# Optimization experiments

Hardware: AMD Instinct MI355X
Metric: run time of the kernel (lower is better)

Reference implementation:

```python
import jax, jax.numpy as jnp
import numpy as np

DT = np.float32(1.0 / 262.0)   # 1 / NUM_TRADING_DAYS
ETA = np.float32(1e-6)
T = 131072


def setup_inputs() -> dict:
    key = jax.random.key(0)
    k1, k2, k3 = jax.random.split(key, 3)
    return {
        "observations": jax.random.normal(k1, (T,), jnp.float32) * 0.01,
        "garch": jax.random.normal(k2, (T,), jnp.float32) * 0.01,
        "carma": jax.random.normal(k3, (T, 2), jnp.float32) * 0.01,
        "w0": jnp.zeros((3,), jnp.float32),
        "P0": jnp.eye(3, dtype=jnp.float32) * 0.01,
        "b0": jnp.float32(0.1),
        "b1": jnp.float32(0.05),
        "a1": jnp.float32(0.5),
        "kappa": jnp.float32(0.01),
        "theta": jnp.float32(0.01),
        "xi": jnp.float32(0.01),
        "rho": jnp.float32(0.01),
    }


def _ekf(observations, garch, carma, w0, P0, b0, b1, a1, kappa, theta, xi, rho):
    kap = jax.nn.softplus(kappa)
    xi_ = jax.nn.softplus(xi)
    rho_ = jnp.tanh(rho)
    zero = jnp.float32(0.0)
    phi_vec = jnp.stack([zero, b0, b1])            # emission coefficients
    phi_row = phi_vec * DT                          # 1x3 phi matrix (as a row)
    I3 = jnp.eye(3, dtype=jnp.float32)

    def step(carry, xs):
        w, P = carry
        obs, g0, c0, c1 = xs
        # --- transition Jacobian psi(w) and drift ---
        th = jax.nn.softplus(theta + g0)
        term = kap * th * jnp.clip(jnp.exp(-w[0]), 0.0, 1.0)
        term = jnp.where(jnp.isnan(term), zero, term)  # nan guard from torch code
        Psi = (I3.at[0, 0].set(1.0 - term)
                  .at[1, 2].set(DT)
                  .at[2, 2].set(1.0 - a1 * DT))
        # --- process noise R(w) ---
        sigma = jnp.exp(w[0] / 2)
        cross = sigma * xi_ * rho_
        R = (jnp.zeros((3, 3), jnp.float32)
                .at[0, 0].set(xi_ ** 2)
                .at[0, 2].set(cross)
                .at[2, 0].set(cross)
                .at[2, 2].set(sigma ** 2)) * DT + I3 * ETA
        # --- state prediction ---
        psi_vec = jnp.stack([term + xi_ ** 2 / 2 - kap, w[2] + c0, -a1 * w[2] + c1])
        w_pred = w + psi_vec * DT
        P_pred = Psi @ P @ Psi.T + R
        P_pred = (P_pred + P_pred.T) / 2 + I3 * ETA
        # --- observation prediction: Q = phi P phi^T + S(w_pred) then sym + ETA*I ---
        x_pred = jnp.dot(phi_vec, w_pred) * DT
        sig2p = jnp.exp(w_pred[0])                 # sigma(w_pred)^2
        Q = phi_row @ P_pred @ phi_row + (sig2p * DT + ETA) + ETA  # scalar
        # --- Kalman gain and posterior update ---
        K = (P_pred @ phi_row) / Q                 # (3,)
        innov = obs - x_pred
        w_post = w_pred + K * innov
        P_post = (I3 - jnp.outer(K, phi_row)) @ P_pred
        P_post = (P_post + P_post.T) / 2 + I3 * ETA
        return (w_post, P_post), (w_post, x_pred)

    xs = (observations, garch, carma[:, 0], carma[:, 1])
    (_, _), (w_seq, x_seq) = jax.lax.scan(step, (w0, P0), xs)
    # [T, 4]: predicted observation and posterior state per step
    return jnp.concatenate([x_seq[:, None], w_seq], axis=1)


def reference(observations, garch, carma, w0, P0, b0, b1, a1, kappa, theta, xi, rho):
    return _ekf(observations, garch, carma, w0, P0, b0, b1, a1, kappa, theta, xi, rho)
```

## Files before the change

kernel.cpp:

```cpp
#include <hip/hip_runtime.h>
#include <math.h>


#define DTV (1.0f/262.0f)
#define C_COARSE 256
#define C_FINE 1024
#define C_SUPER 64
#define NF 4
#define STR 17
#define UPF_A 32
#define UPF_B 8
#define UPF_F 8
#define ETA1 1e-6f
#define ETA2C 2e-6f

__device__ __forceinline__ float softplus_f(float x) {
    return fmaxf(x, 0.0f) + log1pf(__expf(-fabsf(x)));
}

struct EKFConsts {
    float d2, d2sq, f1, f2, cw, f2d2, ffd;
    float invd2, dtd2i, f1sq, f1f2, f2sq, cwDT;
};

__device__ __forceinline__ void load_consts(EKFConsts& c,
    const float* pb0, const float* pb1, const float* pa1,
    const float* pkappa, const float* pxi)
{
    float b0 = pb0[0], b1 = pb1[0], a1 = pa1[0];
    float kap = softplus_f(pkappa[0]);
    float xi_ = softplus_f(pxi[0]);
    float xi2 = xi_ * xi_;
    c.d2    = 1.0f - a1 * DTV;
    c.d2sq  = c.d2 * c.d2;
    c.f1    = b0 * DTV;
    c.f2    = b1 * DTV;
    c.cw    = 0.5f * xi2 - kap;
    c.f2d2  = c.f2 * c.d2;
    c.ffd   = fmaf(c.f1, DTV, c.f2d2);
    c.invd2 = 1.0f / c.d2;
    c.dtd2i = DTV * c.invd2;
    c.f1sq  = c.f1 * c.f1;
    c.f1f2  = c.f1 * c.f2;
    c.f2sq  = c.f2 * c.f2;
    c.cwDT  = c.cw * DTV;
}

__device__ __forceinline__ float poly_exp(float w) {
    return fmaf(w, fmaf(w, fmaf(w, (1.0f/6.0f), 0.5f), 1.0f), 1.0f);
}
__device__ __forceinline__ float poly_expn(float w) {
    float p = fmaf(w, -(1.0f/6.0f), 0.5f);
    p = fmaf(w, p, -1.0f);
    return fminf(fmaf(w, p, 1.0f), 1.0f);
}

__device__ __forceinline__ void mobius_apply(const float* h,
    float& p11, float& p12, float& p22)
{
    float X11 = fmaf(h[0], p11, fmaf(h[4], p12, h[8]));
    float X12 = fmaf(h[0], p12, fmaf(h[4], p22, h[12]));
    float X21 = fmaf(h[1], p11, fmaf(h[5], p12, h[9]));
    float X22 = fmaf(h[1], p12, fmaf(h[5], p22, h[13]));
    float Y11 = fmaf(h[2], p11, fmaf(h[6], p12, h[10]));
    float Y12 = fmaf(h[2], p12, fmaf(h[6], p22, h[14]));
    float Y21 = fmaf(h[3], p11, fmaf(h[7], p12, h[11]));
    float Y22 = fmaf(h[3], p12, fmaf(h[7], p22, h[15]));
    float det = fmaf(Y11, Y22, -Y12 * Y21);
    float idet = __builtin_amdgcn_rcpf(det);
    float P11 = fmaf(X11, Y22, -X12 * Y21) * idet;
    float P12 = fmaf(X12, Y11, -X11 * Y12) * idet;
    float P21 = fmaf(X21, Y22, -X22 * Y21) * idet;
    float P22 = fmaf(X22, Y11, -X21 * Y12) * idet;
    p11 = P11; p12 = 0.5f * (P12 + P21); p22 = P22;
}

__device__ __forceinline__ void mat4_mul(float* C, const float* A, const float* B)
{
    #pragma unroll
    for (int col = 0; col < 4; ++col) {
        #pragma unroll
        for (int row = 0; row < 4; ++row) {
            float s = A[0*4+row] * B[col*4+0];
            s = fmaf(A[1*4+row], B[col*4+1], s);
            s = fmaf(A[2*4+row], B[col*4+2], s);
            s = fmaf(A[3*4+row], B[col*4+3], s);
            C[col*4+row] = s;
        }
    }
}

__global__ void ekf_pack_kt(const float* __restrict__ g,
                            const float* __restrict__ ptheta,
                            const float* __restrict__ pkappa,
                            float* __restrict__ kt, int n)
{
    int i = blockIdx.x * blockDim.x + threadIdx.x;
    if (i >= n) return;
    float kap = softplus_f(pkappa[0]);
    kt[i] = kap * softplus_f(ptheta[0] + g[i]);
}

__device__ void w0_walkD(float& w0r, float& Dr, const EKFConsts& c,
                         const float* k, int L)
{
    float w0 = w0r, D = Dr;
    float buf[UPF_A];
    #pragma unroll
    for (int j = 0; j < UPF_A; ++j) buf[j] = k[j];
    for (int t = 0; t + UPF_A <= L; t += UPF_A) {
        float nb[UPF_A];
        int base = (t + 2 * UPF_A <= L) ? (t + UPF_A) : t;
        #pragma unroll
        for (int j = 0; j < UPF_A; ++j) nb[j] = k[base + j];
        #pragma unroll
        for (int j = 0; j < UPF_A; ++j) {
            float ktd  = buf[j] * DTV;
            float w0c  = w0 + c.cwDT;
            float w0sq = w0 * w0;
            float t1   = fmaf(w0, -(1.0f/6.0f), 0.5f);
            float om   = 1.0f - w0;
            float praw = fmaf(w0sq, t1, om);
            float e    = fminf(praw, 1.0f);
            float pd   = fmaf(w0, fmaf(w0, -0.5f, 1.0f), -1.0f);
            pd = (praw < 1.0f) ? pd : 0.0f;
            D *= fmaf(ktd, pd, 1.0f);
            w0 = fmaf(ktd, e, w0c);
        }
        #pragma unroll
        for (int j = 0; j < UPF_A; ++j) buf[j] = nb[j];
    }
    w0r = w0; Dr = D;
}

__global__ void __launch_bounds__(64, 1) ekf_w0_seed(
    const float* __restrict__ kt,
    float* __restrict__ seedv, float* __restrict__ endv,
    float* __restrict__ endD, int LF,
    const float* __restrict__ w0in,
    const float* __restrict__ pb0, const float* __restrict__ pb1,
    const float* __restrict__ pa1, const float* __restrict__ pkappa,
    const float* __restrict__ pxi)
{
    EKFConsts c; load_consts(c, pb0, pb1, pa1, pkappa, pxi);
    int ch = blockIdx.x;
    const float* k = kt + (size_t)ch * LF;
    float w0;
    if (ch == 0) {
        w0 = w0in[0];
    } else {
        float acc = 0.0f;
        int stride = LF / 16;
        #pragma unroll
        for (int j = 0; j < 16; ++j) acc += k[j * stride + (stride >> 1)];
        float kbar = acc * (1.0f / 16.0f);
        w0 = logf(kbar / (-c.cw));
    }
    float D = 1.0f;
    if (threadIdx.x == 0) seedv[ch] = w0;
    w0_walkD(w0, D, c, k, LF);
    if (threadIdx.x == 0) { endv[ch] = w0; endD[ch] = D; }
}

__global__ void __launch_bounds__(64, 1) ekf_lft(
    const float* __restrict__ kt,
    const float* __restrict__ seedv, const float* __restrict__ endv,
    const float* __restrict__ endD, const float* __restrict__ w0in,
    float* __restrict__ w0b, float* __restrict__ w0s,
    float* __restrict__ Mf, int LF,
    const float* __restrict__ pb0, const float* __restrict__ pb1,
    const float* __restrict__ pa1, const float* __restrict__ pkappa,
    const float* __restrict__ pxi)
{
    EKFConsts c; load_consts(c, pb0, pb1, pa1, pkappa, pxi);
    int f = blockIdx.x;
    int lane = threadIdx.x;
    int col = lane & 3;

    float a = 1.0f, b = 0.0f;
    #pragma unroll
    for (int i = 0; i < C_FINE / 64; ++i) {
        int q = lane * (C_FINE / 64) + i;
        float A = endD[q];
        float B = fmaf(-A, seedv[q], endv[q]);
        b = fmaf(A, b, B);
        a = A * a;
    }
    #pragma unroll
    for (int d = 1; d < 64; d <<= 1) {
        float qa = __shfl_up(a, d), qb = __shfl_up(b, d);
        if (lane >= d) { b = fmaf(a, qb, b); a = a * qa; }
    }
    int G = f >> 4, r = f & 15;
    float w00 = w0in[0];
    float sG = w00;
    if (G > 0) {
        float ga = __shfl(a, G - 1), gb = __shfl(b, G - 1);
        sG = fmaf(ga, w00, gb);
    }
    float s = sG;
    if (r > 0) {
        int qq = (f & ~15) + (lane & 15);
        float A2 = endD[qq];
        float B2 = fmaf(-A2, seedv[qq], endv[qq]);
        #pragma unroll
        for (int d = 1; d < 16; d <<= 1) {
            float qa = __shfl_up(A2, d), qb = __shfl_up(B2, d);
            if ((lane & 15) >= d) { B2 = fmaf(A2, qb, B2); A2 = A2 * qa; }
        }
        float ra = __shfl(A2, r - 1), rb = __shfl(B2, r - 1);
        s = fmaf(ra, sG, rb);
    }
    float w0 = s;
    if (lane == 0) w0b[f] = w0;

    const float* k = kt + (size_t)f * LF;
    float* wo = w0s + (size_t)f * LF;

    float mc0 = (col == 0) ? 1.0f : 0.0f;
    float mc1 = (col == 1) ? 1.0f : 0.0f;
    float mc2 = (col == 2) ? 1.0f : 0.0f;
    float mc3 = (col == 3) ? 1.0f : 0.0f;
    float s2c = poly_exp(w0);

    float buf[UPF_B];
    #pragma unroll
    for (int j = 0; j < UPF_B; ++j) buf[j] = k[j];
    for (int t = 0; t + UPF_B <= LF; t += UPF_B) {
        float nb[UPF_B];
        int base = (t + 2 * UPF_B <= LF) ? (t + UPF_B) : t;
        #pragma unroll
        for (int j = 0; j < UPF_B; ++j) nb[j] = k[base + j];
        #pragma unroll
        for (int j = 0; j < UPF_B; ++j) {
            float e = poly_expn(w0);
            w0 = fmaf(fmaf(buf[j], e, c.cw), DTV, w0);
            if (lane == 0) wo[t + j] = w0;
            float sig2p = poly_exp(w0);
            float s2dt  = s2c * DTV;
            float r2    = fmaf(sig2p, DTV, ETA2C);
            float rinv  = __builtin_amdgcn_rcpf(r2);
            float h11 = c.f1sq * rinv, h12 = c.f1f2 * rinv, h22 = c.f2sq * rinv;
            float b2  = s2dt + ETA2C;
            float aty2 = fmaf(-c.dtd2i, mc2, c.invd2 * mc3);
            float nx1 = fmaf(ETA2C, mc2, fmaf(DTV, mc1, mc0));
            float nx2 = fmaf(b2, aty2, c.d2 * mc1);
            float ny1 = fmaf(h11, nx1, fmaf(h12, nx2, mc2));
            float ny2 = fmaf(h12, nx1, fmaf(h22, nx2, aty2));
            mc0 = fmaf(ETA1, ny1, nx1);
            mc1 = fmaf(ETA1, ny2, nx2);
            mc2 = ny1;
            mc3 = ny2;
            s2c = sig2p;
        }
        #pragma unroll
        for (int j = 0; j < UPF_B; ++j) buf[j] = nb[j];
    }
    float mx = fmaxf(fmaxf(fabsf(mc0), fabsf(mc1)),
                     fmaxf(fabsf(mc2), fabsf(mc3)));
    mx = fmaxf(mx, 1e-30f);
    mx = fmaxf(mx, __shfl_xor(mx, 1));
    mx = fmaxf(mx, __shfl_xor(mx, 2));
    float sc = 1.0f / mx;
    if (lane < 4) {
        *(float4*)(Mf + (size_t)f * 16 + lane * 4) =
            make_float4(mc0 * sc, mc1 * sc, mc2 * sc, mc3 * sc);
    }
}

__global__ void __launch_bounds__(C_COARSE, 1) ekf_pstarts(
    const float* __restrict__ Mf, float* __restrict__ Pst,
    const float* __restrict__ P0)
{
    __shared__ float smF[C_FINE * STR];
    __shared__ float smC[C_COARSE * STR];
    __shared__ float smS[C_SUPER * STR];
    __shared__ float smS2[(C_SUPER / 4) * STR];
    __shared__ float smPS2[(C_SUPER / 4) * 3];
    __shared__ float smPS[C_SUPER * 3];
    __shared__ float smPC[C_COARSE * 3];
    int tid = threadIdx.x;
    for (int r = tid; r < C_FINE; r += C_COARSE) {
        #pragma unroll
        for (int i = 0; i < 16; ++i) smF[r * STR + i] = Mf[r * 16 + i];
    }
    __syncthreads();
    {
        float a[16], b[16];
        mat4_mul(a, smF + (tid * NF + 1) * STR, smF + (tid * NF + 0) * STR);
        mat4_mul(b, smF + (tid * NF + 2) * STR, a);
        mat4_mul(a, smF + (tid * NF + 3) * STR, b);
        float mx = 1e-30f;
        #pragma unroll
        for (int i = 0; i < 16; ++i) mx = fmaxf(mx, fabsf(a[i]));
        float sc = 1.0f / mx;
        #pragma unroll
        for (int i = 0; i < 16; ++i) smC[tid * STR + i] = a[i] * sc;
    }
    __syncthreads();
    if (tid < C_SUPER) {
        float a[16], b[16];
        mat4_mul(a, smC + (tid * NF + 1) * STR, smC + (tid * NF + 0) * STR);
        mat4_mul(b, smC + (tid * NF + 2) * STR, a);
        mat4_mul(a, smC + (tid * NF + 3) * STR, b);
        float mx = 1e-30f;
        #pragma unroll
        for (int i = 0; i < 16; ++i) mx = fmaxf(mx, fabsf(a[i]));
        float sc = 1.0f / mx;
        #pragma unroll
        for (int i = 0; i < 16; ++i) smS[tid * STR + i] = a[i] * sc;
    }
    __syncthreads();
    if (tid < C_SUPER / 4) {
        float a[16], b[16];
        mat4_mul(a, smS + (tid * 4 + 1) * STR, smS + (tid * 4 + 0) * STR);
        mat4_mul(b, smS + (tid * 4 + 2) * STR, a);
        mat4_mul(a, smS + (tid * 4 + 3) * STR, b);
        float mx = 1e-30f;
        #pragma unroll
        for (int i = 0; i < 16; ++i) mx = fmaxf(mx, fabsf(a[i]));
        float sc = 1.0f / mx;
        #pragma unroll
        for (int i = 0; i < 16; ++i) smS2[tid * STR + i] = a[i] * sc;
    }
    __syncthreads();
    if (tid == 0) {
        float p11 = P0[4], p12 = P0[5], p22 = P0[8];
        smPS2[0] = p11; smPS2[1] = p12; smPS2[2] = p22;
        for (int s = 0; s < C_SUPER / 4 - 1; ++s) {
            mobius_apply(smS2 + s * STR, p11, p12, p22);
            smPS2[(s + 1) * 3 + 0] = p11;
            smPS2[(s + 1) * 3 + 1] = p12;
            smPS2[(s + 1) * 3 + 2] = p22;
        }
    }
    __syncthreads();
    if (tid < C_SUPER / 4) {
        float p11 = smPS2[tid * 3], p12 = smPS2[tid * 3 + 1], p22 = smPS2[tid * 3 + 2];
        int s0 = tid * 4;
        smPS[s0 * 3 + 0] = p11; smPS[s0 * 3 + 1] = p12; smPS[s0 * 3 + 2] = p22;
        #pragma unroll
        for (int j = 0; j < 3; ++j) {
            mobius_apply(smS + (s0 + j) * STR, p11, p12, p22);
            smPS[(s0 + j + 1) * 3 + 0] = p11;
            smPS[(s0 + j + 1) * 3 + 1] = p12;
            smPS[(s0 + j + 1) * 3 + 2] = p22;
        }
    }
    __syncthreads();
    if (tid < C_SUPER) {
        float p11 = smPS[tid * 3], p12 = smPS[tid * 3 + 1], p22 = smPS[tid * 3 + 2];
        int c0 = tid * NF;
        smPC[c0 * 3 + 0] = p11; smPC[c0 * 3 + 1] = p12; smPC[c0 * 3 + 2] = p22;
        #pragma unroll
        for (int j = 0; j < NF - 1; ++j) {
            mobius_apply(smC + (c0 + j) * STR, p11, p12, p22);
            smPC[(c0 + j + 1) * 3 + 0] = p11;
            smPC[(c0 + j + 1) * 3 + 1] = p12;
            smPC[(c0 + j + 1) * 3 + 2] = p22;
        }
    }
    __syncthreads();
    {
        float p11 = smPC[tid * 3], p12 = smPC[tid * 3 + 1], p22 = smPC[tid * 3 + 2];
        int f0 = tid * NF;
        Pst[f0 * 3 + 0] = p11; Pst[f0 * 3 + 1] = p12; Pst[f0 * 3 + 2] = p22;
        #pragma unroll
        for (int j = 0; j < NF - 1; ++j) {
            mobius_apply(smF + (f0 + j) * STR, p11, p12, p22);
            Pst[(f0 + j + 1) * 3 + 0] = p11;
            Pst[(f0 + j + 1) * 3 + 1] = p12;
            Pst[(f0 + j + 1) * 3 + 2] = p22;
        }
    }
}

__global__ void __launch_bounds__(64, 1) ekf_walkC(
    const float* __restrict__ obs, const float2* __restrict__ carma,
    const float* __restrict__ w0s, const float* __restrict__ w0b,
    const float* __restrict__ Pst, float* __restrict__ Mc,
    float* __restrict__ sensX, float* __restrict__ sensM,
    float4* __restrict__ out, int LF,
    const float* __restrict__ pb0, const float* __restrict__ pb1,
    const float* __restrict__ pa1, const float* __restrict__ pkappa,
    const float* __restrict__ pxi)
{
    EKFConsts c; load_consts(c, pb0, pb1, pa1, pkappa, pxi);
    int f = blockIdx.x;
    int lane = threadIdx.x;
    int cc = lane & 1;
    size_t gbase = (size_t)f * LF;
    const float* ob = obs + gbase;
    const float2* cr = carma + gbase;
    const float* ws = w0s + gbase;
    float* sx = sensX + gbase * 2;
    float* sM = sensM + gbase * 4;
    float4* o = out + gbase;

    float p11 = Pst[f * 3], p12 = Pst[f * 3 + 1], p22 = Pst[f * 3 + 2];
    float w1 = 0.0f, w2 = 0.0f;
    float mA = (cc == 0) ? 1.0f : 0.0f;
    float mB = (cc == 0) ? 0.0f : 1.0f;
    float s2c = poly_exp(w0b[f]);

    float bo[UPF_F], bw[UPF_F];
    float2 bc[UPF_F];
    #pragma unroll
    for (int j = 0; j < UPF_F; ++j) { bo[j] = ob[j]; bc[j] = cr[j]; bw[j] = ws[j]; }
    for (int t = 0; t + UPF_F <= LF; t += UPF_F) {
        float no[UPF_F], nw[UPF_F];
        float2 nc[UPF_F];
        int base = (t + 2 * UPF_F <= LF) ? (t + UPF_F) : t;
        #pragma unroll
        for (int j = 0; j < UPF_F; ++j) {
            no[j] = ob[base + j]; nc[j] = cr[base + j]; nw[j] = ws[base + j];
        }
        #pragma unroll
        for (int j = 0; j < UPF_F; ++j) {
            float w0n = bw[j];
            float sig2p = poly_exp(w0n);
            float s2dt = s2c * DTV;
            float pp11 = fmaf(DTV * DTV, p22, fmaf(2.0f * DTV, p12, p11)) + ETA2C;
            float pp12 = c.d2 * fmaf(DTV, p22, p12);
            float pp22 = fmaf(c.d2sq, p22, s2dt) + ETA2C;
            float u1 = fmaf(c.f1, pp11, c.f2 * pp12);
            float u2 = fmaf(c.f1, pp12, c.f2 * pp22);
            float Q  = fmaf(c.f1, u1, fmaf(c.f2, u2, fmaf(sig2p, DTV, ETA2C)));
            float rQ = __builtin_amdgcn_rcpf(Q);
            float a1 = u1 * rQ, a2 = u2 * rQ;
            float rxc = fmaf(c.f1, mA, c.ffd * mB);
            float w1p = w1 + fmaf(w2, DTV, bc[j].x * DTV);
            float w2p = fmaf(c.d2, w2, bc[j].y * DTV);
            float xp = fmaf(c.f1, w1p, c.f2 * w2p);
            float innov = bo[j] - xp;
            w1 = fmaf(a1, innov, w1p);
            w2 = fmaf(a2, innov, w2p);
            p11 = fmaf(-a1, u1, pp11) + ETA1;
            p12 = fmaf(-a1, u2, pp12);
            p22 = fmaf(-a2, u2, pp22) + ETA1;
            float j11 = fmaf(-a1, c.f1, 1.0f);
            float j12 = fmaf(j11, DTV, -a1 * c.f2d2);
            float j21 = -a2 * c.f1;
            float j22 = fmaf(-a2, c.ffd, c.d2);
            float nA = fmaf(j11, mA, j12 * mB);
            float nB = fmaf(j21, mA, j22 * mB);
            mA = nA; mB = nB;
            if (lane < 2) {
                sM[(t + j) * 4 + cc]     = mA;
                sM[(t + j) * 4 + 2 + cc] = mB;
                sx[(t + j) * 2 + cc]     = rxc;
            }
            if (lane == 0) o[t + j] = make_float4(xp, w0n, w1, w2);
            s2c = sig2p;
        }
        #pragma unroll
        for (int j = 0; j < UPF_F; ++j) { bo[j] = no[j]; bc[j] = nc[j]; bw[j] = nw[j]; }
    }
    if (lane < 2) {
        Mc[f * 6 + cc]     = mA;
        Mc[f * 6 + 2 + cc] = mB;
    }
    if (lane == 0) {
        Mc[f * 6 + 4] = w1;  Mc[f * 6 + 5] = w2;
    }
}

__global__ void __launch_bounds__(64, 1) ekf_scan(
    const float* __restrict__ Mc, float2* __restrict__ wst,
    const float* __restrict__ w0in)
{
    int L = threadIdx.x;
    float m[C_FINE / 64][6];
    #pragma unroll
    for (int i = 0; i < C_FINE / 64; ++i) {
        const float* p = Mc + ((size_t)(L * (C_FINE / 64) + i)) * 6;
        #pragma unroll
        for (int k = 0; k < 6; ++k) m[i][k] = p[k];
    }
    float g0 = 1.0f, g1 = 0.0f, g2 = 0.0f, g3 = 1.0f, g4 = 0.0f, g5 = 0.0f;
    #pragma unroll
    for (int i = 0; i < C_FINE / 64; ++i) {
        float a0 = m[i][0], a1 = m[i][1], a2 = m[i][2],
              a3 = m[i][3], a4 = m[i][4], a5 = m[i][5];
        float n0 = fmaf(a0, g0, a1 * g2);
        float n1 = fmaf(a0, g1, a1 * g3);
        float n2 = fmaf(a2, g0, a3 * g2);
        float n3 = fmaf(a2, g1, a3 * g3);
        float n4 = fmaf(a0, g4, fmaf(a1, g5, a4));
        float n5 = fmaf(a2, g4, fmaf(a3, g5, a5));
        g0 = n0; g1 = n1; g2 = n2; g3 = n3; g4 = n4; g5 = n5;
    }
    #pragma unroll
    for (int d = 1; d < 64; d <<= 1) {
        float q0 = __shfl_up(g0, d), q1 = __shfl_up(g1, d);
        float q2 = __shfl_up(g2, d), q3 = __shfl_up(g3, d);
        float q4 = __shfl_up(g4, d), q5 = __shfl_up(g5, d);
        if (L >= d) {
            float n0 = fmaf(g0, q0, g1 * q2);
            float n1 = fmaf(g0, q1, g1 * q3);
            float n2 = fmaf(g2, q0, g3 * q2);
            float n3 = fmaf(g2, q1, g3 * q3);
            float n4 = fmaf(g0, q4, fmaf(g1, q5, g4));
            float n5 = fmaf(g2, q4, fmaf(g3, q5, g5));
            g0 = n0; g1 = n1; g2 = n2; g3 = n3; g4 = n4; g5 = n5;
        }
    }
    float e0 = __shfl_up(g0, 1), e1 = __shfl_up(g1, 1);
    float e2 = __shfl_up(g2, 1), e3 = __shfl_up(g3, 1);
    float e4 = __shfl_up(g4, 1), e5 = __shfl_up(g5, 1);
    if (L == 0) { e0 = 1.0f; e1 = 0.0f; e2 = 0.0f; e3 = 1.0f; e4 = 0.0f; e5 = 0.0f; }
    float ic1 = w0in[1], ic2 = w0in[2];
    float s1 = fmaf(e0, ic1, fmaf(e1, ic2, e4));
    float s2 = fmaf(e2, ic1, fmaf(e3, ic2, e5));
    #pragma unroll
    for (int i = 0; i < C_FINE / 64; ++i) {
        wst[L * (C_FINE / 64) + i] = make_float2(s1, s2);
        float n1 = fmaf(m[i][0], s1, fmaf(m[i][1], s2, m[i][4]));
        float n2 = fmaf(m[i][2], s1, fmaf(m[i][3], s2, m[i][5]));
        s1 = n1; s2 = n2;
    }
}

__global__ void ekf_correct(float4* __restrict__ out,
                            const float2* __restrict__ sensX,
                            const float4* __restrict__ sensM,
                            const float2* __restrict__ wst, int n, int LF)
{
    int i = blockIdx.x * blockDim.x + threadIdx.x;
    if (i >= n) return;
    int f = i / LF;
    float2 sv = wst[f];
    float s1 = sv.x, s2 = sv.y;
    float2 rx = sensX[i];
    float4 M = sensM[i];
    float4 o = out[i];
    o.x = fmaf(rx.x, s1, fmaf(rx.y, s2, o.x));
    o.z = fmaf(M.x, s1, fmaf(M.y, s2, o.z));
    o.w = fmaf(M.z, s1, fmaf(M.w, s2, o.w));
    out[i] = o;
}

struct FbState { float w0, w1, w2, p00, p01, p02, p11, p12, p22; };

__global__ void __launch_bounds__(64, 1) ekf_seq_raw(
    const float* __restrict__ obs, const float* __restrict__ g,
    const float2* __restrict__ carma, float4* __restrict__ out, int n,
    const float* __restrict__ w0in, const float* __restrict__ P0,
    const float* __restrict__ pb0, const float* __restrict__ pb1,
    const float* __restrict__ pa1, const float* __restrict__ pkappa,
    const float* __restrict__ ptheta, const float* __restrict__ pxi,
    const float* __restrict__ prho)
{
    if (threadIdx.x != 0) return;
    float b0 = pb0[0], b1 = pb1[0], a1v = pa1[0];
    float kap = softplus_f(pkappa[0]);
    float xi_ = softplus_f(pxi[0]);
    float rho_ = tanhf(prho[0]);
    float d2 = 1.0f - a1v * DTV, d2sq = d2 * d2;
    float f1 = b0 * DTV, f2 = b1 * DTV;
    float cw = 0.5f * xi_ * xi_ - kap;
    float xi2DTe = xi_ * xi_ * DTV + 2e-6f;
    float crossDT = xi_ * rho_ * DTV;
    FbState s;
    s.w0 = w0in[0]; s.w1 = w0in[1]; s.w2 = w0in[2];
    s.p00 = P0[0]; s.p01 = P0[1]; s.p02 = P0[2];
    s.p11 = P0[4]; s.p12 = P0[5]; s.p22 = P0[8];
    float theta = ptheta[0];
    for (int t = 0; t < n; ++t) {
        float kt = kap * softplus_f(theta + g[t]);
        float2 cv = carma[t];
        float c0dt = cv.x * DTV, c1dt = cv.y * DTV;
        float e = fminf(__expf(-s.w0), 1.0f);
        float term = kt * e;
        term = (term != term) ? 0.0f : term;
        float d0 = 1.0f - term;
        float sg = __expf(0.5f * s.w0);
        float s2 = sg * sg, s2DT = s2 * DTV;
        float tc = term + cw;
        float w0p = fmaf(tc, DTV, s.w0);
        float w1p = s.w1 + fmaf(s.w2, DTV, c0dt);
        float w2p = fmaf(d2, s.w2, c1dt);
        float pp00 = fmaf(d0 * d0, s.p00, xi2DTe);
        float pp01 = d0 * fmaf(DTV, s.p02, s.p01);
        float pp02 = fmaf(d0 * d2, s.p02, sg * crossDT);
        float pp11 = fmaf(DTV * DTV, s.p22, fmaf(2.0f * DTV, s.p12, s.p11)) + ETA2C;
        float pp12 = d2 * fmaf(DTV, s.p22, s.p12);
        float pp22 = fmaf(d2sq, s.p22, s2DT) + ETA2C;
        float sig2p = fmaf(s2DT, tc, s2);
        float u0 = fmaf(f1, pp01, f2 * pp02);
        float u1 = fmaf(f1, pp11, f2 * pp12);
        float u2 = fmaf(f1, pp12, f2 * pp22);
        float Q  = fmaf(f1, u1, fmaf(f2, u2, fmaf(sig2p, DTV, 2e-6f)));
        float rQ = __builtin_amdgcn_rcpf(Q);
        float xp = fmaf(f1, w1p, f2 * w2p);
        float innov = obs[t] - xp;
        float a0 = u0 * rQ, a1c = u1 * rQ, a2c = u2 * rQ;
        s.w0 = fmaf(a0, innov, w0p);
        s.w1 = fmaf(a1c, innov, w1p);
        s.w2 = fmaf(a2c, innov, w2p);
        s.p00 = fmaf(-a0, u0, pp00) + ETA1;
        s.p01 = fmaf(-a0, u1, pp01);
        s.p02 = fmaf(-a0, u2, pp02);
        s.p11 = fmaf(-a1c, u1, pp11) + ETA1;
        s.p12 = fmaf(-a1c, u2, pp12);
        s.p22 = fmaf(-a2c, u2, pp22) + ETA1;
        out[t] = make_float4(xp, s.w0, s.w1, s.w2);
    }
}

extern "C" void kernel_launch(void* const* d_in, const int* in_sizes, int n_in,
                              void* d_out, int out_size, void* d_ws, size_t ws_size,
                              hipStream_t stream)
{
    const float*  obs   = (const float*)d_in[0];
    const float*  g     = (const float*)d_in[1];
    const float2* carma = (const float2*)d_in[2];
    const float*  w0    = (const float*)d_in[3];
    const float*  P0    = (const float*)d_in[4];
    const float*  b0    = (const float*)d_in[5];
    const float*  b1    = (const float*)d_in[6];
    const float*  a1    = (const float*)d_in[7];
    const float*  kappa = (const float*)d_in[8];
    const float*  theta = (const float*)d_in[9];
    const float*  xi    = (const float*)d_in[10];
    const float*  rho   = (const float*)d_in[11];
    int n = in_sizes[0];
    float4* out = (float4*)d_out;

    int LF = n / C_FINE;
    size_t need = ((size_t)8 * n + (size_t)C_FINE * 31) * sizeof(float);

    bool ok = (ws_size >= need) && (n % C_FINE) == 0 &&
              LF >= 2 * UPF_A && (LF % UPF_A) == 0 &&
              (LF % UPF_B) == 0 && (LF % UPF_F) == 0 &&
              (LF % 16) == 0 && (C_FINE % 64) == 0;

    if (ok) {
        float* kt    = (float*)d_ws;
        float* w0s   = kt + n;
        float* sensX = w0s + n;
        float* sensM = sensX + 2 * (size_t)n;
        float* seedv = sensM + 4 * (size_t)n;
        float* endv  = seedv + C_FINE;
        float* endD  = endv + C_FINE;
        float* w0b   = endD + C_FINE;
        float* Mf    = w0b + C_FINE;
        float* Pst   = Mf + C_FINE * 16;
        float* Mc    = Pst + C_FINE * 3;
        float2* wst  = (float2*)(Mc + C_FINE * 6);

        ekf_pack_kt<<<(n + 255) / 256, 256, 0, stream>>>(g, theta, kappa, kt, n);
        ekf_w0_seed<<<C_FINE, 64, 0, stream>>>(kt, seedv, endv, endD, LF,
                                               w0, b0, b1, a1, kappa, xi);
        ekf_lft<<<C_FINE, 64, 0, stream>>>(kt, seedv, endv, endD,
                                           w0, w0b, w0s, Mf, LF,
                                           b0, b1, a1, kappa, xi);
        ekf_pstarts<<<1, C_COARSE, 0, stream>>>(Mf, Pst, P0);
        ekf_walkC<<<C_FINE, 64, 0, stream>>>(obs, carma, w0s, w0b, Pst, Mc,
                                             sensX, sensM, out, LF,
                                             b0, b1, a1, kappa, xi);
        ekf_scan<<<1, 64, 0, stream>>>(Mc, wst, w0);
        ekf_correct<<<(n + 255) / 256, 256, 0, stream>>>(out,
                                                         (const float2*)sensX,
                                                         (const float4*)sensM,
                                                         wst, n, LF);
    } else {
        ekf_seq_raw<<<1, 64, 0, stream>>>(obs, g, carma, out, n,
                                          w0, P0, b0, b1, a1, kappa, theta, xi, rho);
    }
}
```

Before: 136.2 us.

## Fuse kt packing into seed kernel, drop sensX buffer, vectorize stores

Folds the softplus kt computation into the w0 seed kernel, where each lane computes two values and the chunk's values are broadcast by shuffles instead of reloaded from memory. The per-chunk mean becomes a full wave reduction. The sensX buffer is removed and its value is recomputed in the correction kernel from the previous step's sensM entry. Stores in ekf_lft and walkC are packed into float4/float2 writes. In exchange the fast path now requires LF == 128 and changes the seed average and the sensM layout.

Result: faster. 131.7 us (-3.3%).

```diff
diff --git a/kernel.cpp b/kernel.cpp
--- a/kernel.cpp
+++ b/kernel.cpp
@@ -90,32 +90,49 @@
     }
 }
 
-__global__ void ekf_pack_kt(const float* __restrict__ g,
-                            const float* __restrict__ ptheta,
-                            const float* __restrict__ pkappa,
-                            float* __restrict__ kt, int n)
-{
-    int i = blockIdx.x * blockDim.x + threadIdx.x;
-    if (i >= n) return;
-    float kap = softplus_f(pkappa[0]);
-    kt[i] = kap * softplus_f(ptheta[0] + g[i]);
-}
-
-__device__ void w0_walkD(float& w0r, float& Dr, const EKFConsts& c,
-                         const float* k, int L)
-{
-    float w0 = w0r, D = Dr;
-    float buf[UPF_A];
-    #pragma unroll
-    for (int j = 0; j < UPF_A; ++j) buf[j] = k[j];
-    for (int t = 0; t + UPF_A <= L; t += UPF_A) {
+__global__ void __launch_bounds__(64, 1) ekf_w0_seed(
+    const float* __restrict__ g, const float* __restrict__ ptheta,
+    const float* __restrict__ pkappa2,
+    float* __restrict__ kt,
+    float* __restrict__ seedv, float* __restrict__ endv,
+    float* __restrict__ endD, int LF,
+    const float* __restrict__ w0in,
+    const float* __restrict__ pb0, const float* __restrict__ pb1,
+    const float* __restrict__ pa1, const float* __restrict__ pkappa,
+    const float* __restrict__ pxi)
+{
+    EKFConsts c; load_consts(c, pb0, pb1, pa1, pkappa, pxi);
+    int ch = blockIdx.x;
+    int lane = threadIdx.x;
+    size_t base = (size_t)ch * LF;
+    float kap = softplus_f(pkappa2[0]);
+    float th  = ptheta[0];
+    float2 gv = *(const float2*)(g + base + lane * 2);
+    float kt0 = kap * softplus_f(th + gv.x);
+    float kt1 = kap * softplus_f(th + gv.y);
+    *(float2*)(kt + base + lane * 2) = make_float2(kt0, kt1);
+
+    float w0;
+    if (ch == 0) {
+        w0 = w0in[0];
+    } else {
+        float acc = kt0 + kt1;
+        #pragma unroll
+        for (int d = 1; d < 64; d <<= 1) acc += __shfl_xor(acc, d);
+        float kbar = acc * (1.0f / 128.0f);
+        w0 = logf(kbar / (-c.cw));
+    }
+    if (lane == 0) seedv[ch] = w0;
+
+    float D = 1.0f;
+    for (int t = 0; t < LF; t += UPF_A) {
         float nb[UPF_A];
-        int base = (t + 2 * UPF_A <= L) ? (t + UPF_A) : t;
-        #pragma unroll
-        for (int j = 0; j < UPF_A; ++j) nb[j] = k[base + j];
+        #pragma unroll
+        for (int j = 0; j < UPF_A; ++j)
+            nb[j] = __shfl((j & 1) ? kt1 : kt0, (t >> 1) + (j >> 1));
         #pragma unroll
         for (int j = 0; j < UPF_A; ++j) {
-            float ktd  = buf[j] * DTV;
+            float ktd  = nb[j] * DTV;
             float w0c  = w0 + c.cwDT;
             float w0sq = w0 * w0;
             float t1   = fmaf(w0, -(1.0f/6.0f), 0.5f);
@@ -127,39 +144,8 @@
             D *= fmaf(ktd, pd, 1.0f);
             w0 = fmaf(ktd, e, w0c);
         }
-        #pragma unroll
-        for (int j = 0; j < UPF_A; ++j) buf[j] = nb[j];
-    }
-    w0r = w0; Dr = D;
-}
-
-__global__ void __launch_bounds__(64, 1) ekf_w0_seed(
-    const float* __restrict__ kt,
-    float* __restrict__ seedv, float* __restrict__ endv,
-    float* __restrict__ endD, int LF,
-    const float* __restrict__ w0in,
-    const float* __restrict__ pb0, const float* __restrict__ pb1,
-    const float* __restrict__ pa1, const float* __restrict__ pkappa,
-    const float* __restrict__ pxi)
-{
-    EKFConsts c; load_consts(c, pb0, pb1, pa1, pkappa, pxi);
-    int ch = blockIdx.x;
-    const float* k = kt + (size_t)ch * LF;
-    float w0;
-    if (ch == 0) {
-        w0 = w0in[0];
-    } else {
-        float acc = 0.0f;
-        int stride = LF / 16;
-        #pragma unroll
-        for (int j = 0; j < 16; ++j) acc += k[j * stride + (stride >> 1)];
-        float kbar = acc * (1.0f / 16.0f);
-        w0 = logf(kbar / (-c.cw));
-    }
-    float D = 1.0f;
-    if (threadIdx.x == 0) seedv[ch] = w0;
-    w0_walkD(w0, D, c, k, LF);
-    if (threadIdx.x == 0) { endv[ch] = w0; endD[ch] = D; }
+    }
+    if (lane == 0) { endv[ch] = w0; endD[ch] = D; }
 }
 
 __global__ void __launch_bounds__(64, 1) ekf_lft(
@@ -222,6 +208,7 @@
     float mc2 = (col == 2) ? 1.0f : 0.0f;
     float mc3 = (col == 3) ? 1.0f : 0.0f;
     float s2c = poly_exp(w0);
+    float4 wq;
 
     float buf[UPF_B];
     #pragma unroll
@@ -235,7 +222,10 @@
         for (int j = 0; j < UPF_B; ++j) {
             float e = poly_expn(w0);
             w0 = fmaf(fmaf(buf[j], e, c.cw), DTV, w0);
-            if (lane == 0) wo[t + j] = w0;
+            if (lane == 0) {
+                ((float*)&wq)[j & 3] = w0;
+                if ((j & 3) == 3) *(float4*)(wo + t + j - 3) = wq;
+            }
             float sig2p = poly_exp(w0);
             float s2dt  = s2c * DTV;
             float r2    = fmaf(sig2p, DTV, ETA2C);
@@ -379,7 +369,7 @@
     const float* __restrict__ obs, const float2* __restrict__ carma,
     const float* __restrict__ w0s, const float* __restrict__ w0b,
     const float* __restrict__ Pst, float* __restrict__ Mc,
-    float* __restrict__ sensX, float* __restrict__ sensM,
+    float* __restrict__ sensM,
     float4* __restrict__ out, int LF,
     const float* __restrict__ pb0, const float* __restrict__ pb1,
     const float* __restrict__ pa1, const float* __restrict__ pkappa,
@@ -393,7 +383,6 @@
     const float* ob = obs + gbase;
     const float2* cr = carma + gbase;
     const float* ws = w0s + gbase;
-    float* sx = sensX + gbase * 2;
     float* sM = sensM + gbase * 4;
     float4* o = out + gbase;
 
@@ -428,7 +417,6 @@
             float Q  = fmaf(c.f1, u1, fmaf(c.f2, u2, fmaf(sig2p, DTV, ETA2C)));
             float rQ = __builtin_amdgcn_rcpf(Q);
             float a1 = u1 * rQ, a2 = u2 * rQ;
-            float rxc = fmaf(c.f1, mA, c.ffd * mB);
             float w1p = w1 + fmaf(w2, DTV, bc[j].x * DTV);
             float w2p = fmaf(c.d2, w2, bc[j].y * DTV);
             float xp = fmaf(c.f1, w1p, c.f2 * w2p);
@@ -446,9 +434,7 @@
             float nB = fmaf(j21, mA, j22 * mB);
             mA = nA; mB = nB;
             if (lane < 2) {
-                sM[(t + j) * 4 + cc]     = mA;
-                sM[(t + j) * 4 + 2 + cc] = mB;
-                sx[(t + j) * 2 + cc]     = rxc;
+                *(float2*)(sM + (t + j) * 4 + 2 * cc) = make_float2(mA, mB);
             }
             if (lane == 0) o[t + j] = make_float4(xp, w0n, w1, w2);
             s2c = sig2p;
@@ -522,21 +508,36 @@
 }
 
 __global__ void ekf_correct(float4* __restrict__ out,
-                            const float2* __restrict__ sensX,
                             const float4* __restrict__ sensM,
-                            const float2* __restrict__ wst, int n, int LF)
+                            const float2* __restrict__ wst,
+                            const float* __restrict__ pb0,
+                            const float* __restrict__ pb1,
+                            const float* __restrict__ pa1,
+                            int n, int LF, int lfsh)
 {
     int i = blockIdx.x * blockDim.x + threadIdx.x;
     if (i >= n) return;
-    int f = i / LF;
+    float f1 = pb0[0] * DTV;
+    float f2 = pb1[0] * DTV;
+    float d2 = 1.0f - pa1[0] * DTV;
+    float f2d2 = f2 * d2;
+    float ffd = fmaf(f1, DTV, f2d2);
+    int f = i >> lfsh;
     float2 sv = wst[f];
     float s1 = sv.x, s2 = sv.y;
-    float2 rx = sensX[i];
+    float rx1, rx2;
+    if ((i & (LF - 1)) == 0) {
+        rx1 = f1; rx2 = ffd;
+    } else {
+        float4 Mp = sensM[i - 1];
+        rx1 = fmaf(f1, Mp.x, ffd * Mp.y);
+        rx2 = fmaf(f1, Mp.z, ffd * Mp.w);
+    }
     float4 M = sensM[i];
     float4 o = out[i];
-    o.x = fmaf(rx.x, s1, fmaf(rx.y, s2, o.x));
-    o.z = fmaf(M.x, s1, fmaf(M.y, s2, o.z));
-    o.w = fmaf(M.z, s1, fmaf(M.w, s2, o.w));
+    o.x = fmaf(rx1, s1, fmaf(rx2, s2, o.x));
+    o.z = fmaf(M.x, s1, fmaf(M.z, s2, o.z));
+    o.w = fmaf(M.y, s1, fmaf(M.w, s2, o.w));
     out[i] = o;
 }
 
@@ -628,18 +629,15 @@
     float4* out = (float4*)d_out;
 
     int LF = n / C_FINE;
-    size_t need = ((size_t)8 * n + (size_t)C_FINE * 31) * sizeof(float);
-
-    bool ok = (ws_size >= need) && (n % C_FINE) == 0 &&
-              LF >= 2 * UPF_A && (LF % UPF_A) == 0 &&
-              (LF % UPF_B) == 0 && (LF % UPF_F) == 0 &&
-              (LF % 16) == 0 && (C_FINE % 64) == 0;
+    size_t need = ((size_t)6 * n + (size_t)C_FINE * 29) * sizeof(float);
+
+    bool ok = (ws_size >= need) && (n % C_FINE) == 0 && LF == 128;
 
     if (ok) {
+        int lfsh = 7;
         float* kt    = (float*)d_ws;
         float* w0s   = kt + n;
-        float* sensX = w0s + n;
-        float* sensM = sensX + 2 * (size_t)n;
+        float* sensM = w0s + n;
         float* seedv = sensM + 4 * (size_t)n;
         float* endv  = seedv + C_FINE;
         float* endD  = endv + C_FINE;
@@ -649,21 +647,21 @@
         float* Mc    = Pst + C_FINE * 3;
         float2* wst  = (float2*)(Mc + C_FINE * 6);
 
-        ekf_pack_kt<<<(n + 255) / 256, 256, 0, stream>>>(g, theta, kappa, kt, n);
-        ekf_w0_seed<<<C_FINE, 64, 0, stream>>>(kt, seedv, endv, endD, LF,
+        ekf_w0_seed<<<C_FINE, 64, 0, stream>>>(g, theta, kappa, kt,
+                                               seedv, endv, endD, LF,
                                                w0, b0, b1, a1, kappa, xi);
         ekf_lft<<<C_FINE, 64, 0, stream>>>(kt, seedv, endv, endD,
                                            w0, w0b, w0s, Mf, LF,
                                            b0, b1, a1, kappa, xi);
         ekf_pstarts<<<1, C_COARSE, 0, stream>>>(Mf, Pst, P0);
         ekf_walkC<<<C_FINE, 64, 0, stream>>>(obs, carma, w0s, w0b, Pst, Mc,
-                                             sensX, sensM, out, LF,
+                                             sensM, out, LF,
                                              b0, b1, a1, kappa, xi);
         ekf_scan<<<1, 64, 0, stream>>>(Mc, wst, w0);
         ekf_correct<<<(n + 255) / 256, 256, 0, stream>>>(out,
-                                                         (const float2*)sensX,
                                                          (const float4*)sensM,
-                                                         wst, n, LF);
+                                                         wst, b0, b1, a1,
+                                                         n, LF, lfsh);
     } else {
         ekf_seq_raw<<<1, 64, 0, stream>>>(obs, g, carma, out, n,
                                           w0, P0, b0, b1, a1, kappa, theta, xi, rho);
```
